# Optimization experiments

Hardware: AMD Instinct MI355X
Metric: run time of the kernel (lower is better)

The kernel has to match this reference:

```python
import jax, jax.numpy as jnp
import numpy as np

N = 100000   # nodes
E = 600000   # edges (before self loops)
D = 128      # dim_latent = H*F
H = 4        # heads
F = 32       # out_feats per head
L = 3        # num GATConv layers (conv_0 + 2)


def setup_inputs() -> dict:
    key = jax.random.key(0)
    ks = jax.random.split(key, 10)
    return {
        "weights": jax.random.normal(ks[0], (N,), jnp.float32),
        "lin_W": jax.random.normal(ks[1], (D, 1), jnp.float32) * 0.1,
        "lin_b": jnp.zeros((D,), jnp.float32),
        "fc_W": jax.random.normal(ks[2], (L, D, D), jnp.float32) * (1.0 / np.sqrt(D)),
        "attn_l": jax.random.normal(ks[3], (L, H, F), jnp.float32) * 0.1,
        "attn_r": jax.random.normal(ks[4], (L, H, F), jnp.float32) * 0.1,
        "conv_b": jnp.zeros((L, D), jnp.float32),
        "pred_W": jax.random.normal(ks[5], (1, D), jnp.float32) * 0.1,
        "pred_b": jnp.zeros((1,), jnp.float32),
        "src": jax.random.randint(ks[6], (E,), 0, N, jnp.int32),
        "dst": jax.random.randint(ks[7], (E,), 0, N, jnp.int32),
    }


def _leaky(x, slope):
    return jnp.where(x >= 0, x, slope * x)


def _gat_conv(x, fc_W, attn_l, attn_r, bias, src, dst):
    # DGL GATConv: bias-free fc, per-head additive attention, edge softmax over dst
    h = (x @ fc_W.T).reshape(N, H, F)                      # [N,H,F]
    el = jnp.sum(h * attn_l[None], axis=-1)                # [N,H]
    er = jnp.sum(h * attn_r[None], axis=-1)                # [N,H]
    e = _leaky(el[src] + er[dst], 0.2)                     # [Etot,H]
    m = jax.ops.segment_max(e, dst, num_segments=N)        # [N,H]
    a = jnp.exp(e - m[dst])                                # [Etot,H]
    s = jax.ops.segment_sum(a, dst, num_segments=N)        # [N,H]
    alpha = a / s[dst]                                     # [Etot,H]
    msg = h[src] * alpha[:, :, None]                       # [Etot,H,F]
    out = jax.ops.segment_sum(msg, dst, num_segments=N)    # [N,H,F]
    out = out + bias.reshape(H, F)[None]
    return out.reshape(N, H * F)


def reference(weights, lin_W, lin_b, fc_W, attn_l, attn_r, conv_b, pred_W, pred_b, src, dst):
    # add self loops (dgl.add_self_loop)
    loop = jnp.arange(N, dtype=src.dtype)
    s_full = jnp.concatenate([src, loop])
    d_full = jnp.concatenate([dst, loop])

    x = weights[:, None] @ lin_W.T + lin_b                 # [N,D]
    for i in range(L):
        if i > 0:
            x = _leaky(x, 0.01)                            # nn.LeakyReLU default
        x = _gat_conv(x, fc_W[i], attn_l[i], attn_r[i], conv_b[i], s_full, d_full)
    logits = x @ pred_W.T + pred_b                         # [N,1]
    return logits
```

## Files before the change

### kernel.cpp

```cpp
#include <hip/hip_runtime.h>
#include <hip/hip_bf16.h>
#include <math.h>


__device__ __forceinline__ float leaky02(float x) {
    return x >= 0.f ? x : 0.2f * x;
}
__device__ __forceinline__ float leaky01(float x) {
    return x >= 0.f ? x : 0.01f * x;
}

__device__ __forceinline__ unsigned short f2bf(float f) {
    unsigned u = __float_as_uint(f);
    unsigned r = u + 0x7FFFu + ((u >> 16) & 1u);
    return (unsigned short)(r >> 16);
}
__device__ __forceinline__ float bf2f(unsigned short s) {
    return __uint_as_float(((unsigned)s) << 16);
}

typedef __attribute__((ext_vector_type(8))) short bf16x8;
typedef __attribute__((ext_vector_type(8))) unsigned short u16x8;
typedef __attribute__((ext_vector_type(4))) float f32x4;

__global__ __launch_bounds__(1024) void prep_kernel(
    int* __restrict__ deg, int N,
    const float* __restrict__ fc_W, const float* __restrict__ attn_l,
    const float* __restrict__ attn_r,
    short* __restrict__ Wh, short* __restrict__ Wl,
    short* __restrict__ Mh, short* __restrict__ Ml,
    const float* __restrict__ lW, const float* __restrict__ lb,
    const float* __restrict__ cb2, const float* __restrict__ pW,
    const float* __restrict__ pb,
    float* __restrict__ c1, float* __restrict__ c2, float* __restrict__ prm)
{
    const int nbi = (N + 1023) >> 10;
    const int b = blockIdx.x;
    const int t = threadIdx.x;

    if (b < nbi) {
        int i = b * 1024 + t;
        if (i < N) deg[i] = 1;
        if (i < 2 * 16384) {
            const float* W = fc_W + 16384;
            int l    = i >> 14;
            int p    = i & 16383;
            int j    = p & 7;
            int lane = (p >> 3) & 63;
            int c    = (p >> 9) & 7;
            int kk   = p >> 12;
            int mr   = lane & 15;
            int quad = lane >> 4;
            int row  = c * 16 + mr;
            int d    = kk * 32 + quad * 8 + j;
            float f = W[(size_t)l * 16384 + row * 128 + d];
            unsigned short hi = f2bf(f);
            Wh[i] = (short)hi;
            Wl[i] = (short)f2bf(f - bf2f(hi));
        }
    } else if (b < nbi + 2) {
        int l = b - nbi;
        const float* W  = fc_W + (size_t)(l + 1) * 16384;
        const float* al = attn_l + (l + 1) * 128;
        const float* ar = attn_r + (l + 1) * 128;
        short* mh = Mh + (size_t)l * 16 * 128;
        short* ml = Ml + (size_t)l * 16 * 128;
        int r = t >> 7;
        int d = t & 127;
        int hh = r & 3;
        const float* av = (r < 4) ? al : ar;
        float s = 0.f;
#pragma unroll
        for (int f = 0; f < 32; ++f)
            s += W[(size_t)(hh * 32 + f) * 128 + d] * av[hh * 32 + f];
        unsigned short hi = f2bf(s);
        mh[r * 128 + d] = (short)hi;
        ml[r * 128 + d] = (short)f2bf(s - bf2f(hi));
        mh[(r + 8) * 128 + d] = 0;
        ml[(r + 8) * 128 + d] = 0;
    } else {
        __shared__ float sh1[128], sh2[128], sh3[128], sh4[128], sh5[128];
        const float* W0 = fc_W;
        const float* al = attn_l;
        const float* ar = attn_r;
        int j = t >> 3, sub = t & 7;
        float s1 = 0.f, s2 = 0.f;
        int d0 = sub * 16;
#pragma unroll
        for (int k = 0; k < 16; ++k) {
            float wv = W0[j * 128 + d0 + k];
            s1 += lW[d0 + k] * wv;
            s2 += lb[d0 + k] * wv;
        }
#pragma unroll
        for (int m = 1; m <= 4; m <<= 1) {
            s1 += __shfl_xor(s1, m, 64);
            s2 += __shfl_xor(s2, m, 64);
        }
        if (sub == 0) {
            c1[j] = s1; c2[j] = s2;
            sh1[j] = s1 * al[j]; sh2[j] = s2 * al[j];
            sh3[j] = s1 * ar[j]; sh4[j] = s2 * ar[j];
            sh5[j] = cb2[j] * pW[j];
        }
        __syncthreads();
        if (t < 4) {
            float p = 0.f, q = 0.f, r = 0.f, s = 0.f;
            for (int f = 0; f < 32; ++f) {
                p += sh1[t * 32 + f]; q += sh2[t * 32 + f];
                r += sh3[t * 32 + f]; s += sh4[t * 32 + f];
            }
            prm[t] = p; prm[4 + t] = q; prm[8 + t] = r; prm[12 + t] = s;
        }
        if (t == 0) {
            float cs = 0.f;
            for (int k = 0; k < 128; ++k) cs += sh5[k];
            prm[16] = cs + pb[0];
        }
    }
}

__global__ __launch_bounds__(256) void deg_count_slot_kernel(
    const int* __restrict__ dst, int* __restrict__ deg,
    int* __restrict__ slot, int E)
{
    int i = blockIdx.x * 256 + threadIdx.x;
    if (i < E) slot[i] = atomicAdd(&deg[dst[i]], 1);
}

#define SCAN_TILE 1024

__global__ __launch_bounds__(256) void scanA_kernel(
    const int* __restrict__ deg, int* __restrict__ bsum, int N)
{
    __shared__ int ws[4];
    int b = blockIdx.x, t = threadIdx.x;
    int base = b * SCAN_TILE + t * 4;
    int s = 0;
#pragma unroll
    for (int k = 0; k < 4; ++k) {
        int i = base + k;
        if (i < N) s += deg[i];
    }
#pragma unroll
    for (int m = 32; m >= 1; m >>= 1) s += __shfl_xor(s, m, 64);
    if ((t & 63) == 0) ws[t >> 6] = s;
    __syncthreads();
    if (t == 0) bsum[b] = ws[0] + ws[1] + ws[2] + ws[3];
}

__global__ __launch_bounds__(1024) void scanB_kernel(
    int* __restrict__ bsum, int* __restrict__ bpre, int* __restrict__ rowp,
    int NB, int N)
{
    __shared__ int sh[1024];
    int t = threadIdx.x;
    int v = (t < NB) ? bsum[t] : 0;
    sh[t] = v;
    __syncthreads();
    for (int off = 1; off < 1024; off <<= 1) {
        int u = (t >= off) ? sh[t - off] : 0;
        __syncthreads();
        sh[t] += u;
        __syncthreads();
    }
    if (t < NB) bpre[t] = sh[t] - v;
    if (t == 1023) rowp[N] = sh[1023];
}

__global__ __launch_bounds__(256) void scanC_kernel(
    const int* __restrict__ deg, const int* __restrict__ bpre,
    int* __restrict__ rowp, int* __restrict__ col, int N)
{
    __shared__ int sh[256];
    int b = blockIdx.x, t = threadIdx.x;
    int base = b * SCAN_TILE + t * 4;
    int v[4];
#pragma unroll
    for (int k = 0; k < 4; ++k) {
        int i = base + k;
        v[k] = (i < N) ? deg[i] : 0;
    }
    int tsum = v[0] + v[1] + v[2] + v[3];
    sh[t] = tsum;
    __syncthreads();
    for (int off = 1; off < 256; off <<= 1) {
        int u = (t >= off) ? sh[t - off] : 0;
        __syncthreads();
        sh[t] += u;
        __syncthreads();
    }
    int pre = bpre[b] + sh[t] - tsum;
#pragma unroll
    for (int k = 0; k < 4; ++k) {
        int i = base + k;
        if (i < N) {
            rowp[i] = pre;
            col[pre] = i;
        }
        pre += v[k];
    }
}

__global__ __launch_bounds__(256) void scatter2_kernel(
    const int* __restrict__ src, const int* __restrict__ dst,
    const int* __restrict__ slot, const int* __restrict__ rowp,
    int* __restrict__ col, int E)
{
    int i = blockIdx.x * 256 + threadIdx.x;
    if (i < E) col[rowp[dst[i]] + slot[i]] = src[i];
}

__global__ __launch_bounds__(256) void agg0_kernel(
    const float* __restrict__ w, const float* __restrict__ c1,
    const float* __restrict__ c2, const float* __restrict__ prm,
    const int* __restrict__ rowp, const int* __restrict__ col,
    const float* __restrict__ bias, unsigned short* __restrict__ xout, int N)
{
    const int lane = threadIdx.x & 63;
    const int q    = lane >> 4;
    const int l16  = lane & 15;
    const int v    = blockIdx.x * 16 + (threadIdx.x >> 6) * 4 + q;
    if (v >= N) return;

    const int r0 = rowp[v], r1 = rowp[v + 1];
    const int head = l16 >> 2;
    const int e4   = l16 & 3;
    const int f0   = l16 * 8;
    const float pl = prm[head],     ql = prm[4 + head];
    const float pr = prm[8 + head], qr = prm[12 + head];

    const float wv  = w[v];
    const float erq = wv * pr + qr;
    const float mref = leaky02(wv * pl + ql + erq);

    float S = 0.f, Sw = 0.f;
    for (int j = r0 + e4; j < r1; j += 4) {
        int u = col[j];
        float wu = w[u];
        float e = leaky02(wu * pl + ql + erq);
        float d = fminf(e - mref, 80.f);
        float p = __expf(d);
        S += p; Sw += p * wu;
    }
    S  += __shfl_xor(S, 1, 64);  S  += __shfl_xor(S, 2, 64);
    Sw += __shfl_xor(Sw, 1, 64); Sw += __shfl_xor(Sw, 2, 64);
    const float t = Sw / S;

    float4 a0 = *reinterpret_cast<const float4*>(&c1[f0]);
    float4 a1 = *reinterpret_cast<const float4*>(&c1[f0 + 4]);
    float4 g0 = *reinterpret_cast<const float4*>(&c2[f0]);
    float4 g1 = *reinterpret_cast<const float4*>(&c2[f0 + 4]);
    float4 b0 = *reinterpret_cast<const float4*>(&bias[f0]);
    float4 b1 = *reinterpret_cast<const float4*>(&bias[f0 + 4]);
    const float aa[8] = {a0.x, a0.y, a0.z, a0.w, a1.x, a1.y, a1.z, a1.w};
    const float gg[8] = {g0.x, g0.y, g0.z, g0.w, g1.x, g1.y, g1.z, g1.w};
    const float bb[8] = {b0.x, b0.y, b0.z, b0.w, b1.x, b1.y, b1.z, b1.w};

    u16x8 o;
#pragma unroll
    for (int k = 0; k < 8; ++k)
        o[k] = f2bf(leaky01(t * aa[k] + gg[k] + bb[k]));
    *reinterpret_cast<u16x8*>(&xout[(size_t)v * 128 + f0]) = o;
}

__global__ __launch_bounds__(256) void gemm_mfma_kernel(
    const unsigned short* __restrict__ xb, const short* __restrict__ Wh,
    const short* __restrict__ Wl, const short* __restrict__ Mh,
    const short* __restrict__ Ml, unsigned short* __restrict__ hb,
    float* __restrict__ el, float* __restrict__ er,
    const float* __restrict__ pW, float* __restrict__ yel,
    int N, int mode)
{
    const int lane = threadIdx.x & 63;
    const int wv   = threadIdx.x >> 6;
    const int m0   = blockIdx.x * 128 + wv * 32;
    const int mr   = lane & 15;
    const int quad = lane >> 4;

    int r0 = m0 + mr;      if (r0 > N - 1) r0 = N - 1;
    int r1 = m0 + 16 + mr; if (r1 > N - 1) r1 = N - 1;
    const unsigned short* xp0 = xb + (size_t)r0 * 128 + quad * 8;
    const unsigned short* xp1 = xb + (size_t)r1 * 128 + quad * 8;

    f32x4 acc0[8], acc1[8], acce0, acce1;
#pragma unroll
    for (int c = 0; c < 8; ++c) {
        acc0[c] = (f32x4){0.f, 0.f, 0.f, 0.f};
        acc1[c] = (f32x4){0.f, 0.f, 0.f, 0.f};
    }
    acce0 = (f32x4){0.f, 0.f, 0.f, 0.f};
    acce1 = (f32x4){0.f, 0.f, 0.f, 0.f};

#pragma unroll
    for (int kk = 0; kk < 4; ++kk) {
        bf16x8 a0 = *reinterpret_cast<const bf16x8*>(xp0 + kk * 32);
        bf16x8 a1 = *reinterpret_cast<const bf16x8*>(xp1 + kk * 32);

        const int kb = kk * 32 + quad * 8;
        bf16x8 bh[8], bl[8];
#pragma unroll
        for (int c = 0; c < 8; ++c) {
            const size_t wo = (size_t)((kk * 8 + c) * 64 + lane) * 8;
            bh[c] = *reinterpret_cast<const bf16x8*>(Wh + wo);
            bl[c] = *reinterpret_cast<const bf16x8*>(Wl + wo);
        }
        bf16x8 eh = *reinterpret_cast<const bf16x8*>(Mh + (size_t)mr * 128 + kb);
        bf16x8 eo = *reinterpret_cast<const bf16x8*>(Ml + (size_t)mr * 128 + kb);
#pragma unroll
        for (int c = 0; c < 8; ++c) {
            acc0[c] = __builtin_amdgcn_mfma_f32_16x16x32_bf16(a0, bh[c], acc0[c], 0, 0, 0);
            acc0[c] = __builtin_amdgcn_mfma_f32_16x16x32_bf16(a0, bl[c], acc0[c], 0, 0, 0);
            acc1[c] = __builtin_amdgcn_mfma_f32_16x16x32_bf16(a1, bh[c], acc1[c], 0, 0, 0);
            acc1[c] = __builtin_amdgcn_mfma_f32_16x16x32_bf16(a1, bl[c], acc1[c], 0, 0, 0);
        }
        acce0 = __builtin_amdgcn_mfma_f32_16x16x32_bf16(a0, eh, acce0, 0, 0, 0);
        acce0 = __builtin_amdgcn_mfma_f32_16x16x32_bf16(a0, eo, acce0, 0, 0, 0);
        acce1 = __builtin_amdgcn_mfma_f32_16x16x32_bf16(a1, eh, acce1, 0, 0, 0);
        acce1 = __builtin_amdgcn_mfma_f32_16x16x32_bf16(a1, eo, acce1, 0, 0, 0);
    }

    if (mode == 0) {
#pragma unroll
        for (int i = 0; i < 4; ++i) {
            int rowA = m0 + quad * 4 + i;
            if (rowA < N) {
                unsigned short* hp = hb + (size_t)rowA * 128 + mr;
#pragma unroll
                for (int c = 0; c < 8; ++c) hp[c * 16] = f2bf(acc0[c][i]);
                if (mr < 4)       el[(size_t)rowA * 4 + mr]       = acce0[i];
                else if (mr < 8)  er[(size_t)rowA * 4 + (mr - 4)] = acce0[i];
            }
            int rowB = m0 + 16 + quad * 4 + i;
            if (rowB < N) {
                unsigned short* hp = hb + (size_t)rowB * 128 + mr;
#pragma unroll
                for (int c = 0; c < 8; ++c) hp[c * 16] = f2bf(acc1[c][i]);
                if (mr < 4)       el[(size_t)rowB * 4 + mr]       = acce1[i];
                else if (mr < 8)  er[(size_t)rowB * 4 + (mr - 4)] = acce1[i];
            }
        }
    } else {
        float pw[8];
#pragma unroll
        for (int c = 0; c < 8; ++c) pw[c] = pW[mr + c * 16];
#pragma unroll
        for (int i = 0; i < 4; ++i) {
            int rowA = m0 + quad * 4 + i;
            {
                float y[4];
#pragma unroll
                for (int h = 0; h < 4; ++h)
                    y[h] = acc0[2 * h][i] * pw[2 * h] + acc0[2 * h + 1][i] * pw[2 * h + 1];
#pragma unroll
                for (int d = 1; d < 16; d <<= 1) {
#pragma unroll
                    for (int h = 0; h < 4; ++h) y[h] += __shfl_xor(y[h], d, 64);
                }
                if (rowA < N) {
                    if (mr < 4) {
                        float2 o; o.x = y[mr]; o.y = acce0[i];
                        *reinterpret_cast<float2*>(&yel[(size_t)rowA * 8 + mr * 2]) = o;
                    } else if (mr < 8) {
                        er[(size_t)rowA * 4 + (mr - 4)] = acce0[i];
                    }
                }
            }
            int rowB = m0 + 16 + quad * 4 + i;
            {
                float y[4];
#pragma unroll
                for (int h = 0; h < 4; ++h)
                    y[h] = acc1[2 * h][i] * pw[2 * h] + acc1[2 * h + 1][i] * pw[2 * h + 1];
#pragma unroll
                for (int d = 1; d < 16; d <<= 1) {
#pragma unroll
                    for (int h = 0; h < 4; ++h) y[h] += __shfl_xor(y[h], d, 64);
                }
                if (rowB < N) {
                    if (mr < 4) {
                        float2 o; o.x = y[mr]; o.y = acce1[i];
                        *reinterpret_cast<float2*>(&yel[(size_t)rowB * 8 + mr * 2]) = o;
                    } else if (mr < 8) {
                        er[(size_t)rowB * 4 + (mr - 4)] = acce1[i];
                    }
                }
            }
        }
    }
}

__global__ __launch_bounds__(256) void agg_mid_kernel(
    const unsigned short* __restrict__ hb, const float* __restrict__ el,
    const float* __restrict__ er, const int* __restrict__ rowp,
    const int* __restrict__ col, const float* __restrict__ bias,
    unsigned short* __restrict__ xout, int N)
{
    const int lane = threadIdx.x & 63;
    const int q    = lane >> 4;
    const int l16  = lane & 15;
    const int v    = blockIdx.x * 16 + (threadIdx.x >> 6) * 4 + q;
    if (v >= N) return;

    const int r0 = rowp[v], r1 = rowp[v + 1];
    const int head = l16 >> 2;
    const int f0   = l16 * 8;
    const float erq = er[(size_t)v * 4 + head];
    const float el_self = el[(size_t)v * 4 + head];
    const float mref = leaky02(el_self + erq);

    float s = 0.f;
    float acc[8];
#pragma unroll
    for (int k = 0; k < 8; ++k) acc[k] = 0.f;

    float elA = el_self;
    u16x8 hvA = *reinterpret_cast<const u16x8*>(&hb[(size_t)v * 128 + f0]);
    int jB = (r0 + 1 < r1) ? r0 + 1 : r1 - 1;
    int uB = col[jB];
    float elB = el[(size_t)uB * 4 + head];
    u16x8 hvB = *reinterpret_cast<const u16x8*>(&hb[(size_t)uB * 128 + f0]);

    for (int j = r0; j < r1; j += 2) {
        int jA2 = (j + 2 < r1) ? j + 2 : r1 - 1;
        int uA2 = col[jA2];
        float elA2 = el[(size_t)uA2 * 4 + head];
        u16x8 hvA2 = *reinterpret_cast<const u16x8*>(&hb[(size_t)uA2 * 128 + f0]);

        {
            float e = leaky02(elA + erq);
            float d = fminf(e - mref, 80.f);
            float p = __expf(d);
            s += p;
#pragma unroll
            for (int k = 0; k < 8; ++k) acc[k] += p * bf2f(hvA[k]);
        }

        if (j + 1 < r1) {
            int jB2 = (j + 3 < r1) ? j + 3 : r1 - 1;
            int uB2 = col[jB2];
            float elB2 = el[(size_t)uB2 * 4 + head];
            u16x8 hvB2 = *reinterpret_cast<const u16x8*>(&hb[(size_t)uB2 * 128 + f0]);

            float e = leaky02(elB + erq);
            float d = fminf(e - mref, 80.f);
            float p = __expf(d);
            s += p;
#pragma unroll
            for (int k = 0; k < 8; ++k) acc[k] += p * bf2f(hvB[k]);

            elB = elB2; hvB = hvB2;
        }
        elA = elA2; hvA = hvA2;
    }
    const float is = 1.f / s;

    float4 b0 = *reinterpret_cast<const float4*>(&bias[f0]);
    float4 b1 = *reinterpret_cast<const float4*>(&bias[f0 + 4]);
    const float bb[8] = {b0.x, b0.y, b0.z, b0.w, b1.x, b1.y, b1.z, b1.w};

    u16x8 o;
#pragma unroll
    for (int k = 0; k < 8; ++k) o[k] = f2bf(leaky01(acc[k] * is + bb[k]));
    *reinterpret_cast<u16x8*>(&xout[(size_t)v * 128 + f0]) = o;
}

__global__ __launch_bounds__(256) void agg2_kernel(
    const float* __restrict__ yel, const float* __restrict__ er,
    const int* __restrict__ rowp, const int* __restrict__ col,
    const float* __restrict__ prm, float* __restrict__ logits, int N)
{
    const int lane = threadIdx.x & 63;
    const int q    = lane >> 4;
    const int l16  = lane & 15;
    const int v    = blockIdx.x * 16 + (threadIdx.x >> 6) * 4 + q;
    if (v >= N) return;

    const int r0 = rowp[v], r1 = rowp[v + 1];
    const int head = l16 >> 2;
    const int e4   = l16 & 3;
    const float erq = er[(size_t)v * 4 + head];

    float2 selfy = *reinterpret_cast<const float2*>(&yel[(size_t)v * 8 + head * 2]);
    const float mref = leaky02(selfy.y + erq);

    float S = 0.f, A = 0.f;
    for (int j = r0 + e4; j < r1; j += 4) {
        int u = col[j];
        float2 c = *reinterpret_cast<const float2*>(&yel[(size_t)u * 8 + head * 2]);
        float e = leaky02(c.y + erq);
        float d = fminf(e - mref, 80.f);
        float p = __expf(d);
        S += p; A += p * c.x;
    }
    S += __shfl_xor(S, 1, 64); S += __shfl_xor(S, 2, 64);
    A += __shfl_xor(A, 1, 64); A += __shfl_xor(A, 2, 64);
    float part = A / S;
    part += __shfl_xor(part, 4, 64);
    part += __shfl_xor(part, 8, 64);
    if (l16 == 0) logits[v] = part + prm[16];
}

extern "C" void kernel_launch(void* const* d_in, const int* in_sizes, int n_in,
                              void* d_out, int out_size, void* d_ws, size_t ws_size,
                              hipStream_t stream)
{
    const float* weights = (const float*)d_in[0];
    const float* lin_W   = (const float*)d_in[1];
    const float* lin_b   = (const float*)d_in[2];
    const float* fc_W    = (const float*)d_in[3];
    const float* attn_l  = (const float*)d_in[4];
    const float* attn_r  = (const float*)d_in[5];
    const float* conv_b  = (const float*)d_in[6];
    const float* pred_W  = (const float*)d_in[7];
    const float* pred_b  = (const float*)d_in[8];
    const int*   src     = (const int*)d_in[9];
    const int*   dst     = (const int*)d_in[10];

    const int N = in_sizes[0];
    const int E = in_sizes[9];
    const int NB = (N + SCAN_TILE - 1) / SCAN_TILE;
    const int NBI = (N + 1023) / 1024;

    unsigned short* xb = (unsigned short*)d_ws;
    unsigned short* hb = xb + (size_t)N * 128;
    float* el  = (float*)(hb + (size_t)N * 128);
    float* er  = el + (size_t)N * 4;
    float* yel = er + (size_t)N * 4;
    float* c1  = yel + (size_t)N * 8;
    float* c2  = c1 + 128;
    float* prm = c2 + 128;
    short* Whs = (short*)(prm + 32);
    short* Wls = Whs + 2 * 16384;
    short* Mhs = Wls + 2 * 16384;
    short* Mls = Mhs + 2 * 2048;
    int*   deg  = (int*)(Mls + 2 * 2048);
    int*   rowp = deg + N;
    int*   slot = rowp + (N + 1);
    int*   col  = slot + E;
    int*   bsum = col + (E + N);
    int*   bpre = bsum + NB;

    prep_kernel<<<NBI + 3, 1024, 0, stream>>>(
        deg, N, fc_W, attn_l, attn_r, Whs, Wls, Mhs, Mls,
        lin_W, lin_b, conv_b + 2 * 128, pred_W, pred_b, c1, c2, prm);

    deg_count_slot_kernel<<<(E + 255) / 256, 256, 0, stream>>>(dst, deg, slot, E);
    scanA_kernel<<<NB, 256, 0, stream>>>(deg, bsum, N);
    scanB_kernel<<<1, 1024, 0, stream>>>(bsum, bpre, rowp, NB, N);
    scanC_kernel<<<NB, 256, 0, stream>>>(deg, bpre, rowp, col, N);
    scatter2_kernel<<<(E + 255) / 256, 256, 0, stream>>>(src, dst, slot, rowp, col, E);

    agg0_kernel<<<(N + 15) / 16, 256, 0, stream>>>(
        weights, c1, c2, prm, rowp, col, conv_b, xb, N);

    gemm_mfma_kernel<<<(N + 127) / 128, 256, 0, stream>>>(
        xb, Whs, Wls, Mhs, Mls, hb, el, er, pred_W, yel, N, 0);
    agg_mid_kernel<<<(N + 15) / 16, 256, 0, stream>>>(
        hb, el, er, rowp, col, conv_b + 128, xb, N);

    gemm_mfma_kernel<<<(N + 127) / 128, 256, 0, stream>>>(
        xb, Whs + 16384, Wls + 16384, Mhs + 2048, Mls + 2048,
        hb, el, er, pred_W, yel, N, 1);
    agg2_kernel<<<(N + 15) / 16, 256, 0, stream>>>(
        yel, er, rowp, col, prm, (float*)d_out, N);
}
```

Before: 251.8 us.

## Fuse edge aggregation into following GEMM and collapse scan into single pass

Each aggregation stage now writes its bf16 node features into a shared-memory tile, and the same block immediately runs the MFMA projection for the next layer. This removes the global round trip of the intermediate feature matrix and two kernel launches. The three-kernel prefix scan is replaced by one kernel in which each 1024-node block claims its output base with an atomic counter. CSR row offsets are therefore no longer ordered by vertex, so row ends are computed from deg instead of rowp[v+1]. The trade-off is that each block now aggregates 128 nodes serially across 8 passes before its GEMM can start, which may reduce latency hiding.

```diff
diff --git a/kernel.cpp b/kernel.cpp
--- a/kernel.cpp
+++ b/kernel.cpp
@@ -32,11 +32,13 @@
     const float* __restrict__ lW, const float* __restrict__ lb,
     const float* __restrict__ cb2, const float* __restrict__ pW,
     const float* __restrict__ pb,
-    float* __restrict__ c1, float* __restrict__ c2, float* __restrict__ prm)
+    float* __restrict__ c1, float* __restrict__ c2, float* __restrict__ prm,
+    int* __restrict__ base_ctr)
 {
     const int nbi = (N + 1023) >> 10;
     const int b = blockIdx.x;
     const int t = threadIdx.x;
+    if (b == 0 && t == 0) *base_ctr = 0;
 
     if (b < nbi) {
         int i = b * 1024 + t;
@@ -128,34 +130,15 @@
     if (i < E) slot[i] = atomicAdd(&deg[dst[i]], 1);
 }
 
-#define SCAN_TILE 1024
-
-__global__ __launch_bounds__(256) void scanA_kernel(
-    const int* __restrict__ deg, int* __restrict__ bsum, int N)
-{
-    __shared__ int ws[4];
+__global__ __launch_bounds__(1024) void scan_kernel(
+    const int* __restrict__ deg, int* __restrict__ base_ctr,
+    int* __restrict__ rowp, int* __restrict__ col, int N)
+{
+    __shared__ int sh[1024];
+    __shared__ int sbase;
     int b = blockIdx.x, t = threadIdx.x;
-    int base = b * SCAN_TILE + t * 4;
-    int s = 0;
-#pragma unroll
-    for (int k = 0; k < 4; ++k) {
-        int i = base + k;
-        if (i < N) s += deg[i];
-    }
-#pragma unroll
-    for (int m = 32; m >= 1; m >>= 1) s += __shfl_xor(s, m, 64);
-    if ((t & 63) == 0) ws[t >> 6] = s;
-    __syncthreads();
-    if (t == 0) bsum[b] = ws[0] + ws[1] + ws[2] + ws[3];
-}
-
-__global__ __launch_bounds__(1024) void scanB_kernel(
-    int* __restrict__ bsum, int* __restrict__ bpre, int* __restrict__ rowp,
-    int NB, int N)
-{
-    __shared__ int sh[1024];
-    int t = threadIdx.x;
-    int v = (t < NB) ? bsum[t] : 0;
+    int i = b * 1024 + t;
+    int v = (i < N) ? deg[i] : 0;
     sh[t] = v;
     __syncthreads();
     for (int off = 1; off < 1024; off <<= 1) {
@@ -164,41 +147,12 @@
         sh[t] += u;
         __syncthreads();
     }
-    if (t < NB) bpre[t] = sh[t] - v;
-    if (t == 1023) rowp[N] = sh[1023];
-}
-
-__global__ __launch_bounds__(256) void scanC_kernel(
-    const int* __restrict__ deg, const int* __restrict__ bpre,
-    int* __restrict__ rowp, int* __restrict__ col, int N)
-{
-    __shared__ int sh[256];
-    int b = blockIdx.x, t = threadIdx.x;
-    int base = b * SCAN_TILE + t * 4;
-    int v[4];
-#pragma unroll
-    for (int k = 0; k < 4; ++k) {
-        int i = base + k;
-        v[k] = (i < N) ? deg[i] : 0;
-    }
-    int tsum = v[0] + v[1] + v[2] + v[3];
-    sh[t] = tsum;
+    if (t == 1023) sbase = atomicAdd(base_ctr, sh[1023]);
     __syncthreads();
-    for (int off = 1; off < 256; off <<= 1) {
-        int u = (t >= off) ? sh[t - off] : 0;
-        __syncthreads();
-        sh[t] += u;
-        __syncthreads();
-    }
-    int pre = bpre[b] + sh[t] - tsum;
-#pragma unroll
-    for (int k = 0; k < 4; ++k) {
-        int i = base + k;
-        if (i < N) {
-            rowp[i] = pre;
-            col[pre] = i;
-        }
-        pre += v[k];
+    int pre = sbase + sh[t] - v;
+    if (i < N) {
+        rowp[i] = pre;
+        col[pre] = i;
     }
 }
 
@@ -211,11 +165,319 @@
     if (i < E) col[rowp[dst[i]] + slot[i]] = src[i];
 }
 
-__global__ __launch_bounds__(256) void agg0_kernel(
+__global__ __launch_bounds__(256) void l0g1_kernel(
     const float* __restrict__ w, const float* __restrict__ c1,
     const float* __restrict__ c2, const float* __restrict__ prm,
-    const int* __restrict__ rowp, const int* __restrict__ col,
-    const float* __restrict__ bias, unsigned short* __restrict__ xout, int N)
+    const int* __restrict__ rowp, const int* __restrict__ deg,
+    const int* __restrict__ col, const float* __restrict__ bias,
+    const short* __restrict__ Wh, const short* __restrict__ Wl,
+    const short* __restrict__ Mh, const short* __restrict__ Ml,
+    unsigned short* __restrict__ hb, float* __restrict__ el,
+    float* __restrict__ er, int N)
+{
+    __shared__ unsigned short xs[128][136];
+    const int t    = threadIdx.x;
+    const int lane = t & 63;
+    const int wv   = t >> 6;
+    const int q    = lane >> 4;
+    const int l16  = lane & 15;
+    const int head = l16 >> 2;
+    const int e4   = l16 & 3;
+    const int f0   = l16 * 8;
+    const int vbase = blockIdx.x * 128;
+
+    const float pl = prm[head],     ql = prm[4 + head];
+    const float pr = prm[8 + head], qr = prm[12 + head];
+    float4 a0v = *reinterpret_cast<const float4*>(&c1[f0]);
+    float4 a1v = *reinterpret_cast<const float4*>(&c1[f0 + 4]);
+    float4 g0v = *reinterpret_cast<const float4*>(&c2[f0]);
+    float4 g1v = *reinterpret_cast<const float4*>(&c2[f0 + 4]);
+    float4 b0v = *reinterpret_cast<const float4*>(&bias[f0]);
+    float4 b1v = *reinterpret_cast<const float4*>(&bias[f0 + 4]);
+    const float aa[8] = {a0v.x, a0v.y, a0v.z, a0v.w, a1v.x, a1v.y, a1v.z, a1v.w};
+    const float gg[8] = {g0v.x, g0v.y, g0v.z, g0v.w, g1v.x, g1v.y, g1v.z, g1v.w};
+    const float bb[8] = {b0v.x, b0v.y, b0v.z, b0v.w, b1v.x, b1v.y, b1v.z, b1v.w};
+
+#pragma unroll
+    for (int p = 0; p < 8; ++p) {
+        const int lr = p * 16 + wv * 4 + q;
+        const int v  = vbase + lr;
+        u16x8 o;
+        if (v < N) {
+            const int r0 = rowp[v];
+            const int r1 = r0 + deg[v];
+            const float wvx  = w[v];
+            const float erq  = wvx * pr + qr;
+            const float mref = leaky02(wvx * pl + ql + erq);
+            float S = 0.f, Sw = 0.f;
+            for (int j = r0 + e4; j < r1; j += 4) {
+                int u = col[j];
+                float wu = w[u];
+                float e = leaky02(wu * pl + ql + erq);
+                float d = fminf(e - mref, 80.f);
+                float pp = __expf(d);
+                S += pp; Sw += pp * wu;
+            }
+            S  += __shfl_xor(S, 1, 64);  S  += __shfl_xor(S, 2, 64);
+            Sw += __shfl_xor(Sw, 1, 64); Sw += __shfl_xor(Sw, 2, 64);
+            const float tt = Sw / S;
+#pragma unroll
+            for (int k = 0; k < 8; ++k)
+                o[k] = f2bf(leaky01(tt * aa[k] + gg[k] + bb[k]));
+        } else {
+#pragma unroll
+            for (int k = 0; k < 8; ++k) o[k] = 0;
+        }
+        *reinterpret_cast<u16x8*>(&xs[lr][f0]) = o;
+    }
+    __syncthreads();
+
+    const int m0   = vbase + wv * 32;
+    const int mr   = lane & 15;
+    const int quad = lane >> 4;
+
+    f32x4 acc0[8], acc1[8], acce0, acce1;
+#pragma unroll
+    for (int c = 0; c < 8; ++c) {
+        acc0[c] = (f32x4){0.f, 0.f, 0.f, 0.f};
+        acc1[c] = (f32x4){0.f, 0.f, 0.f, 0.f};
+    }
+    acce0 = (f32x4){0.f, 0.f, 0.f, 0.f};
+    acce1 = (f32x4){0.f, 0.f, 0.f, 0.f};
+
+#pragma unroll
+    for (int kk = 0; kk < 4; ++kk) {
+        bf16x8 a0 = *reinterpret_cast<const bf16x8*>(&xs[wv * 32 + mr][quad * 8 + kk * 32]);
+        bf16x8 a1 = *reinterpret_cast<const bf16x8*>(&xs[wv * 32 + 16 + mr][quad * 8 + kk * 32]);
+
+        const int kb = kk * 32 + quad * 8;
+        bf16x8 bh[8], bl[8];
+#pragma unroll
+        for (int c = 0; c < 8; ++c) {
+            const size_t wo = (size_t)((kk * 8 + c) * 64 + lane) * 8;
+            bh[c] = *reinterpret_cast<const bf16x8*>(Wh + wo);
+            bl[c] = *reinterpret_cast<const bf16x8*>(Wl + wo);
+        }
+        bf16x8 eh = *reinterpret_cast<const bf16x8*>(Mh + (size_t)mr * 128 + kb);
+        bf16x8 eo = *reinterpret_cast<const bf16x8*>(Ml + (size_t)mr * 128 + kb);
+#pragma unroll
+        for (int c = 0; c < 8; ++c) {
+            acc0[c] = __builtin_amdgcn_mfma_f32_16x16x32_bf16(a0, bh[c], acc0[c], 0, 0, 0);
+            acc0[c] = __builtin_amdgcn_mfma_f32_16x16x32_bf16(a0, bl[c], acc0[c], 0, 0, 0);
+            acc1[c] = __builtin_amdgcn_mfma_f32_16x16x32_bf16(a1, bh[c], acc1[c], 0, 0, 0);
+            acc1[c] = __builtin_amdgcn_mfma_f32_16x16x32_bf16(a1, bl[c], acc1[c], 0, 0, 0);
+        }
+        acce0 = __builtin_amdgcn_mfma_f32_16x16x32_bf16(a0, eh, acce0, 0, 0, 0);
+        acce0 = __builtin_amdgcn_mfma_f32_16x16x32_bf16(a0, eo, acce0, 0, 0, 0);
+        acce1 = __builtin_amdgcn_mfma_f32_16x16x32_bf16(a1, eh, acce1, 0, 0, 0);
+        acce1 = __builtin_amdgcn_mfma_f32_16x16x32_bf16(a1, eo, acce1, 0, 0, 0);
+    }
+
+#pragma unroll
+    for (int i = 0; i < 4; ++i) {
+        int rowA = m0 + quad * 4 + i;
+        if (rowA < N) {
+            unsigned short* hp = hb + (size_t)rowA * 128 + mr;
+#pragma unroll
+            for (int c = 0; c < 8; ++c) hp[c * 16] = f2bf(acc0[c][i]);
+            if (mr < 4)       el[(size_t)rowA * 4 + mr]       = acce0[i];
+            else if (mr < 8)  er[(size_t)rowA * 4 + (mr - 4)] = acce0[i];
+        }
+        int rowB = m0 + 16 + quad * 4 + i;
+        if (rowB < N) {
+            unsigned short* hp = hb + (size_t)rowB * 128 + mr;
+#pragma unroll
+            for (int c = 0; c < 8; ++c) hp[c * 16] = f2bf(acc1[c][i]);
+            if (mr < 4)       el[(size_t)rowB * 4 + mr]       = acce1[i];
+            else if (mr < 8)  er[(size_t)rowB * 4 + (mr - 4)] = acce1[i];
+        }
+    }
+}
+
+__global__ __launch_bounds__(256) void midg2_kernel(
+    const unsigned short* __restrict__ hb, const float* __restrict__ el,
+    float* __restrict__ er, const int* __restrict__ rowp,
+    const int* __restrict__ deg, const int* __restrict__ col,
+    const float* __restrict__ bias,
+    const short* __restrict__ Wh, const short* __restrict__ Wl,
+    const short* __restrict__ Mh, const short* __restrict__ Ml,
+    const float* __restrict__ pW, float* __restrict__ yel, int N)
+{
+    __shared__ unsigned short xs[128][136];
+    const int t    = threadIdx.x;
+    const int lane = t & 63;
+    const int wv   = t >> 6;
+    const int q    = lane >> 4;
+    const int l16  = lane & 15;
+    const int head = l16 >> 2;
+    const int f0   = l16 * 8;
+    const int vbase = blockIdx.x * 128;
+
+    float4 b0v = *reinterpret_cast<const float4*>(&bias[f0]);
+    float4 b1v = *reinterpret_cast<const float4*>(&bias[f0 + 4]);
+    const float bb[8] = {b0v.x, b0v.y, b0v.z, b0v.w, b1v.x, b1v.y, b1v.z, b1v.w};
+
+#pragma unroll
+    for (int p = 0; p < 8; ++p) {
+        const int lr = p * 16 + wv * 4 + q;
+        const int v  = vbase + lr;
+        u16x8 o;
+        if (v < N) {
+            const int r0 = rowp[v];
+            const int r1 = r0 + deg[v];
+            const float erq = er[(size_t)v * 4 + head];
+            const float el_self = el[(size_t)v * 4 + head];
+            const float mref = leaky02(el_self + erq);
+
+            float s = 0.f;
+            float acc[8];
+#pragma unroll
+            for (int k = 0; k < 8; ++k) acc[k] = 0.f;
+
+            float elA = el_self;
+            u16x8 hvA = *reinterpret_cast<const u16x8*>(&hb[(size_t)v * 128 + f0]);
+            int jB = (r0 + 1 < r1) ? r0 + 1 : r1 - 1;
+            int uB = col[jB];
+            float elB = el[(size_t)uB * 4 + head];
+            u16x8 hvB = *reinterpret_cast<const u16x8*>(&hb[(size_t)uB * 128 + f0]);
+
+            for (int j = r0; j < r1; j += 2) {
+                int jA2 = (j + 2 < r1) ? j + 2 : r1 - 1;
+                int uA2 = col[jA2];
+                float elA2 = el[(size_t)uA2 * 4 + head];
+                u16x8 hvA2 = *reinterpret_cast<const u16x8*>(&hb[(size_t)uA2 * 128 + f0]);
+
+                {
+                    float e = leaky02(elA + erq);
+                    float d = fminf(e - mref, 80.f);
+                    float pp = __expf(d);
+                    s += pp;
+#pragma unroll
+                    for (int k = 0; k < 8; ++k) acc[k] += pp * bf2f(hvA[k]);
+                }
+                if (j + 1 < r1) {
+                    int jB2 = (j + 3 < r1) ? j + 3 : r1 - 1;
+                    int uB2 = col[jB2];
+                    float elB2 = el[(size_t)uB2 * 4 + head];
+                    u16x8 hvB2 = *reinterpret_cast<const u16x8*>(&hb[(size_t)uB2 * 128 + f0]);
+
+                    float e = leaky02(elB + erq);
+                    float d = fminf(e - mref, 80.f);
+                    float pp = __expf(d);
+                    s += pp;
+#pragma unroll
+                    for (int k = 0; k < 8; ++k) acc[k] += pp * bf2f(hvB[k]);
+
+                    elB = elB2; hvB = hvB2;
+                }
+                elA = elA2; hvA = hvA2;
+            }
+            const float is = 1.f / s;
+#pragma unroll
+            for (int k = 0; k < 8; ++k)
+                o[k] = f2bf(leaky01(acc[k] * is + bb[k]));
+        } else {
+#pragma unroll
+            for (int k = 0; k < 8; ++k) o[k] = 0;
+        }
+        *reinterpret_cast<u16x8*>(&xs[lr][f0]) = o;
+    }
+    __syncthreads();
+
+    const int m0   = vbase + wv * 32;
+    const int mr   = lane & 15;
+    const int quad = lane >> 4;
+
+    f32x4 acc0[8], acc1[8], acce0, acce1;
+#pragma unroll
+    for (int c = 0; c < 8; ++c) {
+        acc0[c] = (f32x4){0.f, 0.f, 0.f, 0.f};
+        acc1[c] = (f32x4){0.f, 0.f, 0.f, 0.f};
+    }
+    acce0 = (f32x4){0.f, 0.f, 0.f, 0.f};
+    acce1 = (f32x4){0.f, 0.f, 0.f, 0.f};
+
+#pragma unroll
+    for (int kk = 0; kk < 4; ++kk) {
+        bf16x8 a0 = *reinterpret_cast<const bf16x8*>(&xs[wv * 32 + mr][quad * 8 + kk * 32]);
+        bf16x8 a1 = *reinterpret_cast<const bf16x8*>(&xs[wv * 32 + 16 + mr][quad * 8 + kk * 32]);
+
+        const int kb = kk * 32 + quad * 8;
+        bf16x8 bh[8], bl[8];
+#pragma unroll
+        for (int c = 0; c < 8; ++c) {
+            const size_t wo = (size_t)((kk * 8 + c) * 64 + lane) * 8;
+            bh[c] = *reinterpret_cast<const bf16x8*>(Wh + wo);
+            bl[c] = *reinterpret_cast<const bf16x8*>(Wl + wo);
+        }
+        bf16x8 eh = *reinterpret_cast<const bf16x8*>(Mh + (size_t)mr * 128 + kb);
+        bf16x8 eo = *reinterpret_cast<const bf16x8*>(Ml + (size_t)mr * 128 + kb);
+#pragma unroll
+        for (int c = 0; c < 8; ++c) {
+            acc0[c] = __builtin_amdgcn_mfma_f32_16x16x32_bf16(a0, bh[c], acc0[c], 0, 0, 0);
+            acc0[c] = __builtin_amdgcn_mfma_f32_16x16x32_bf16(a0, bl[c], acc0[c], 0, 0, 0);
+            acc1[c] = __builtin_amdgcn_mfma_f32_16x16x32_bf16(a1, bh[c], acc1[c], 0, 0, 0);
+            acc1[c] = __builtin_amdgcn_mfma_f32_16x16x32_bf16(a1, bl[c], acc1[c], 0, 0, 0);
+        }
+        acce0 = __builtin_amdgcn_mfma_f32_16x16x32_bf16(a0, eh, acce0, 0, 0, 0);
+        acce0 = __builtin_amdgcn_mfma_f32_16x16x32_bf16(a0, eo, acce0, 0, 0, 0);
+        acce1 = __builtin_amdgcn_mfma_f32_16x16x32_bf16(a1, eh, acce1, 0, 0, 0);
+        acce1 = __builtin_amdgcn_mfma_f32_16x16x32_bf16(a1, eo, acce1, 0, 0, 0);
+    }
+
+    float pw[8];
+#pragma unroll
+    for (int c = 0; c < 8; ++c) pw[c] = pW[mr + c * 16];
+#pragma unroll
+    for (int i = 0; i < 4; ++i) {
+        int rowA = m0 + quad * 4 + i;
+        {
+            float y[4];
+#pragma unroll
+            for (int h = 0; h < 4; ++h)
+                y[h] = acc0[2 * h][i] * pw[2 * h] + acc0[2 * h + 1][i] * pw[2 * h + 1];
+#pragma unroll
+            for (int d = 1; d < 16; d <<= 1) {
+#pragma unroll
+                for (int h = 0; h < 4; ++h) y[h] += __shfl_xor(y[h], d, 64);
+            }
+            if (rowA < N) {
+                if (mr < 4) {
+                    float2 o; o.x = y[mr]; o.y = acce0[i];
+                    *reinterpret_cast<float2*>(&yel[(size_t)rowA * 8 + mr * 2]) = o;
+                } else if (mr < 8) {
+                    er[(size_t)rowA * 4 + (mr - 4)] = acce0[i];
+                }
+            }
+        }
+        int rowB = m0 + 16 + quad * 4 + i;
+        {
+            float y[4];
+#pragma unroll
+            for (int h = 0; h < 4; ++h)
+                y[h] = acc1[2 * h][i] * pw[2 * h] + acc1[2 * h + 1][i] * pw[2 * h + 1];
+#pragma unroll
+            for (int d = 1; d < 16; d <<= 1) {
+#pragma unroll
+                for (int h = 0; h < 4; ++h) y[h] += __shfl_xor(y[h], d, 64);
+            }
+            if (rowB < N) {
+                if (mr < 4) {
+                    float2 o; o.x = y[mr]; o.y = acce1[i];
+                    *reinterpret_cast<float2*>(&yel[(size_t)rowB * 8 + mr * 2]) = o;
+                } else if (mr < 8) {
+                    er[(size_t)rowB * 4 + (mr - 4)] = acce1[i];
+                }
+            }
+        }
+    }
+}
+
+__global__ __launch_bounds__(256) void agg2_kernel(
+    const float* __restrict__ yel, const float* __restrict__ er,
+    const int* __restrict__ rowp, const int* __restrict__ deg,
+    const int* __restrict__ col, const float* __restrict__ prm,
+    float* __restrict__ logits, int N)
 {
     const int lane = threadIdx.x & 63;
     const int q    = lane >> 4;
@@ -223,260 +485,8 @@
     const int v    = blockIdx.x * 16 + (threadIdx.x >> 6) * 4 + q;
     if (v >= N) return;
 
-    const int r0 = rowp[v], r1 = rowp[v + 1];
-    const int head = l16 >> 2;
-    const int e4   = l16 & 3;
-    const int f0   = l16 * 8;
-    const float pl = prm[head],     ql = prm[4 + head];
-    const float pr = prm[8 + head], qr = prm[12 + head];
-
-    const float wv  = w[v];
-    const float erq = wv * pr + qr;
-    const float mref = leaky02(wv * pl + ql + erq);
-
-    float S = 0.f, Sw = 0.f;
-    for (int j = r0 + e4; j < r1; j += 4) {
-        int u = col[j];
-        float wu = w[u];
-        float e = leaky02(wu * pl + ql + erq);
-        float d = fminf(e - mref, 80.f);
-        float p = __expf(d);
-        S += p; Sw += p * wu;
-    }
-    S  += __shfl_xor(S, 1, 64);  S  += __shfl_xor(S, 2, 64);
-    Sw += __shfl_xor(Sw, 1, 64); Sw += __shfl_xor(Sw, 2, 64);
-    const float t = Sw / S;
-
-    float4 a0 = *reinterpret_cast<const float4*>(&c1[f0]);
-    float4 a1 = *reinterpret_cast<const float4*>(&c1[f0 + 4]);
-    float4 g0 = *reinterpret_cast<const float4*>(&c2[f0]);
-    float4 g1 = *reinterpret_cast<const float4*>(&c2[f0 + 4]);
-    float4 b0 = *reinterpret_cast<const float4*>(&bias[f0]);
-    float4 b1 = *reinterpret_cast<const float4*>(&bias[f0 + 4]);
-    const float aa[8] = {a0.x, a0.y, a0.z, a0.w, a1.x, a1.y, a1.z, a1.w};
-    const float gg[8] = {g0.x, g0.y, g0.z, g0.w, g1.x, g1.y, g1.z, g1.w};
-    const float bb[8] = {b0.x, b0.y, b0.z, b0.w, b1.x, b1.y, b1.z, b1.w};
-
-    u16x8 o;
-#pragma unroll
-    for (int k = 0; k < 8; ++k)
-        o[k] = f2bf(leaky01(t * aa[k] + gg[k] + bb[k]));
-    *reinterpret_cast<u16x8*>(&xout[(size_t)v * 128 + f0]) = o;
-}
-
-__global__ __launch_bounds__(256) void gemm_mfma_kernel(
-    const unsigned short* __restrict__ xb, const short* __restrict__ Wh,
-    const short* __restrict__ Wl, const short* __restrict__ Mh,
-    const short* __restrict__ Ml, unsigned short* __restrict__ hb,
-    float* __restrict__ el, float* __restrict__ er,
-    const float* __restrict__ pW, float* __restrict__ yel,
-    int N, int mode)
-{
-    const int lane = threadIdx.x & 63;
-    const int wv   = threadIdx.x >> 6;
-    const int m0   = blockIdx.x * 128 + wv * 32;
-    const int mr   = lane & 15;
-    const int quad = lane >> 4;
-
-    int r0 = m0 + mr;      if (r0 > N - 1) r0 = N - 1;
-    int r1 = m0 + 16 + mr; if (r1 > N - 1) r1 = N - 1;
-    const unsigned short* xp0 = xb + (size_t)r0 * 128 + quad * 8;
-    const unsigned short* xp1 = xb + (size_t)r1 * 128 + quad * 8;
-
-    f32x4 acc0[8], acc1[8], acce0, acce1;
-#pragma unroll
-    for (int c = 0; c < 8; ++c) {
-        acc0[c] = (f32x4){0.f, 0.f, 0.f, 0.f};
-        acc1[c] = (f32x4){0.f, 0.f, 0.f, 0.f};
-    }
-    acce0 = (f32x4){0.f, 0.f, 0.f, 0.f};
-    acce1 = (f32x4){0.f, 0.f, 0.f, 0.f};
-
-#pragma unroll
-    for (int kk = 0; kk < 4; ++kk) {
-        bf16x8 a0 = *reinterpret_cast<const bf16x8*>(xp0 + kk * 32);
-        bf16x8 a1 = *reinterpret_cast<const bf16x8*>(xp1 + kk * 32);
-
-        const int kb = kk * 32 + quad * 8;
-        bf16x8 bh[8], bl[8];
-#pragma unroll
-        for (int c = 0; c < 8; ++c) {
-            const size_t wo = (size_t)((kk * 8 + c) * 64 + lane) * 8;
-            bh[c] = *reinterpret_cast<const bf16x8*>(Wh + wo);
-            bl[c] = *reinterpret_cast<const bf16x8*>(Wl + wo);
-        }
-        bf16x8 eh = *reinterpret_cast<const bf16x8*>(Mh + (size_t)mr * 128 + kb);
-        bf16x8 eo = *reinterpret_cast<const bf16x8*>(Ml + (size_t)mr * 128 + kb);
-#pragma unroll
-        for (int c = 0; c < 8; ++c) {
-            acc0[c] = __builtin_amdgcn_mfma_f32_16x16x32_bf16(a0, bh[c], acc0[c], 0, 0, 0);
-            acc0[c] = __builtin_amdgcn_mfma_f32_16x16x32_bf16(a0, bl[c], acc0[c], 0, 0, 0);
-            acc1[c] = __builtin_amdgcn_mfma_f32_16x16x32_bf16(a1, bh[c], acc1[c], 0, 0, 0);
-            acc1[c] = __builtin_amdgcn_mfma_f32_16x16x32_bf16(a1, bl[c], acc1[c], 0, 0, 0);
-        }
-        acce0 = __builtin_amdgcn_mfma_f32_16x16x32_bf16(a0, eh, acce0, 0, 0, 0);
-        acce0 = __builtin_amdgcn_mfma_f32_16x16x32_bf16(a0, eo, acce0, 0, 0, 0);
-        acce1 = __builtin_amdgcn_mfma_f32_16x16x32_bf16(a1, eh, acce1, 0, 0, 0);
-        acce1 = __builtin_amdgcn_mfma_f32_16x16x32_bf16(a1, eo, acce1, 0, 0, 0);
-    }
-
-    if (mode == 0) {
-#pragma unroll
-        for (int i = 0; i < 4; ++i) {
-            int rowA = m0 + quad * 4 + i;
-            if (rowA < N) {
-                unsigned short* hp = hb + (size_t)rowA * 128 + mr;
-#pragma unroll
-                for (int c = 0; c < 8; ++c) hp[c * 16] = f2bf(acc0[c][i]);
-                if (mr < 4)       el[(size_t)rowA * 4 + mr]       = acce0[i];
-                else if (mr < 8)  er[(size_t)rowA * 4 + (mr - 4)] = acce0[i];
-            }
-            int rowB = m0 + 16 + quad * 4 + i;
-            if (rowB < N) {
-                unsigned short* hp = hb + (size_t)rowB * 128 + mr;
-#pragma unroll
-                for (int c = 0; c < 8; ++c) hp[c * 16] = f2bf(acc1[c][i]);
-                if (mr < 4)       el[(size_t)rowB * 4 + mr]       = acce1[i];
-                else if (mr < 8)  er[(size_t)rowB * 4 + (mr - 4)] = acce1[i];
-            }
-        }
-    } else {
-        float pw[8];
-#pragma unroll
-        for (int c = 0; c < 8; ++c) pw[c] = pW[mr + c * 16];
-#pragma unroll
-        for (int i = 0; i < 4; ++i) {
-            int rowA = m0 + quad * 4 + i;
-            {
-                float y[4];
-#pragma unroll
-                for (int h = 0; h < 4; ++h)
-                    y[h] = acc0[2 * h][i] * pw[2 * h] + acc0[2 * h + 1][i] * pw[2 * h + 1];
-#pragma unroll
-                for (int d = 1; d < 16; d <<= 1) {
-#pragma unroll
-                    for (int h = 0; h < 4; ++h) y[h] += __shfl_xor(y[h], d, 64);
-                }
-                if (rowA < N) {
-                    if (mr < 4) {
-                        float2 o; o.x = y[mr]; o.y = acce0[i];
-                        *reinterpret_cast<float2*>(&yel[(size_t)rowA * 8 + mr * 2]) = o;
-                    } else if (mr < 8) {
-                        er[(size_t)rowA * 4 + (mr - 4)] = acce0[i];
-                    }
-                }
-            }
-            int rowB = m0 + 16 + quad * 4 + i;
-            {
-                float y[4];
-#pragma unroll
-                for (int h = 0; h < 4; ++h)
-                    y[h] = acc1[2 * h][i] * pw[2 * h] + acc1[2 * h + 1][i] * pw[2 * h + 1];
-#pragma unroll
-                for (int d = 1; d < 16; d <<= 1) {
-#pragma unroll
-                    for (int h = 0; h < 4; ++h) y[h] += __shfl_xor(y[h], d, 64);
-                }
-                if (rowB < N) {
-                    if (mr < 4) {
-                        float2 o; o.x = y[mr]; o.y = acce1[i];
-                        *reinterpret_cast<float2*>(&yel[(size_t)rowB * 8 + mr * 2]) = o;
-                    } else if (mr < 8) {
-                        er[(size_t)rowB * 4 + (mr - 4)] = acce1[i];
-                    }
-                }
-            }
-        }
-    }
-}
-
-__global__ __launch_bounds__(256) void agg_mid_kernel(
-    const unsigned short* __restrict__ hb, const float* __restrict__ el,
-    const float* __restrict__ er, const int* __restrict__ rowp,
-    const int* __restrict__ col, const float* __restrict__ bias,
-    unsigned short* __restrict__ xout, int N)
-{
-    const int lane = threadIdx.x & 63;
-    const int q    = lane >> 4;
-    const int l16  = lane & 15;
-    const int v    = blockIdx.x * 16 + (threadIdx.x >> 6) * 4 + q;
-    if (v >= N) return;
-
-    const int r0 = rowp[v], r1 = rowp[v + 1];
-    const int head = l16 >> 2;
-    const int f0   = l16 * 8;
-    const float erq = er[(size_t)v * 4 + head];
-    const float el_self = el[(size_t)v * 4 + head];
-    const float mref = leaky02(el_self + erq);
-
-    float s = 0.f;
-    float acc[8];
-#pragma unroll
-    for (int k = 0; k < 8; ++k) acc[k] = 0.f;
-
-    float elA = el_self;
-    u16x8 hvA = *reinterpret_cast<const u16x8*>(&hb[(size_t)v * 128 + f0]);
-    int jB = (r0 + 1 < r1) ? r0 + 1 : r1 - 1;
-    int uB = col[jB];
-    float elB = el[(size_t)uB * 4 + head];
-    u16x8 hvB = *reinterpret_cast<const u16x8*>(&hb[(size_t)uB * 128 + f0]);
-
-    for (int j = r0; j < r1; j += 2) {
-        int jA2 = (j + 2 < r1) ? j + 2 : r1 - 1;
-        int uA2 = col[jA2];
-        float elA2 = el[(size_t)uA2 * 4 + head];
-        u16x8 hvA2 = *reinterpret_cast<const u16x8*>(&hb[(size_t)uA2 * 128 + f0]);
-
-        {
-            float e = leaky02(elA + erq);
-            float d = fminf(e - mref, 80.f);
-            float p = __expf(d);
-            s += p;
-#pragma unroll
-            for (int k = 0; k < 8; ++k) acc[k] += p * bf2f(hvA[k]);
-        }
-
-        if (j + 1 < r1) {
-            int jB2 = (j + 3 < r1) ? j + 3 : r1 - 1;
-            int uB2 = col[jB2];
-            float elB2 = el[(size_t)uB2 * 4 + head];
-            u16x8 hvB2 = *reinterpret_cast<const u16x8*>(&hb[(size_t)uB2 * 128 + f0]);
-
-            float e = leaky02(elB + erq);
-            float d = fminf(e - mref, 80.f);
-            float p = __expf(d);
-            s += p;
-#pragma unroll
-            for (int k = 0; k < 8; ++k) acc[k] += p * bf2f(hvB[k]);
-
-            elB = elB2; hvB = hvB2;
-        }
-        elA = elA2; hvA = hvA2;
-    }
-    const float is = 1.f / s;
-
-    float4 b0 = *reinterpret_cast<const float4*>(&bias[f0]);
-    float4 b1 = *reinterpret_cast<const float4*>(&bias[f0 + 4]);
-    const float bb[8] = {b0.x, b0.y, b0.z, b0.w, b1.x, b1.y, b1.z, b1.w};
-
-    u16x8 o;
-#pragma unroll
-    for (int k = 0; k < 8; ++k) o[k] = f2bf(leaky01(acc[k] * is + bb[k]));
-    *reinterpret_cast<u16x8*>(&xout[(size_t)v * 128 + f0]) = o;
-}
-
-__global__ __launch_bounds__(256) void agg2_kernel(
-    const float* __restrict__ yel, const float* __restrict__ er,
-    const int* __restrict__ rowp, const int* __restrict__ col,
-    const float* __restrict__ prm, float* __restrict__ logits, int N)
-{
-    const int lane = threadIdx.x & 63;
-    const int q    = lane >> 4;
-    const int l16  = lane & 15;
-    const int v    = blockIdx.x * 16 + (threadIdx.x >> 6) * 4 + q;
-    if (v >= N) return;
-
-    const int r0 = rowp[v], r1 = rowp[v + 1];
+    const int r0 = rowp[v];
+    const int r1 = r0 + deg[v];
     const int head = l16 >> 2;
     const int e4   = l16 & 3;
     const float erq = er[(size_t)v * 4 + head];
@@ -519,11 +529,9 @@
 
     const int N = in_sizes[0];
     const int E = in_sizes[9];
-    const int NB = (N + SCAN_TILE - 1) / SCAN_TILE;
-    const int NBI = (N + 1023) / 1024;
-
-    unsigned short* xb = (unsigned short*)d_ws;
-    unsigned short* hb = xb + (size_t)N * 128;
+    const int NB1024 = (N + 1023) / 1024;
+
+    unsigned short* hb = (unsigned short*)d_ws;
     float* el  = (float*)(hb + (size_t)N * 128);
     float* er  = el + (size_t)N * 4;
     float* yel = er + (size_t)N * 4;
@@ -538,30 +546,26 @@
     int*   rowp = deg + N;
     int*   slot = rowp + (N + 1);
     int*   col  = slot + E;
-    int*   bsum = col + (E + N);
-    int*   bpre = bsum + NB;
-
-    prep_kernel<<<NBI + 3, 1024, 0, stream>>>(
+    int*   bctr = col + (E + N);
+
+    prep_kernel<<<NB1024 + 3, 1024, 0, stream>>>(
         deg, N, fc_W, attn_l, attn_r, Whs, Wls, Mhs, Mls,
-        lin_W, lin_b, conv_b + 2 * 128, pred_W, pred_b, c1, c2, prm);
+        lin_W, lin_b, conv_b + 2 * 128, pred_W, pred_b, c1, c2, prm, bctr);
 
     deg_count_slot_kernel<<<(E + 255) / 256, 256, 0, stream>>>(dst, deg, slot, E);
-    scanA_kernel<<<NB, 256, 0, stream>>>(deg, bsum, N);
-    scanB_kernel<<<1, 1024, 0, stream>>>(bsum, bpre, rowp, NB, N);
-    scanC_kernel<<<NB, 256, 0, stream>>>(deg, bpre, rowp, col, N);
+
+    scan_kernel<<<NB1024, 1024, 0, stream>>>(deg, bctr, rowp, col, N);
+
     scatter2_kernel<<<(E + 255) / 256, 256, 0, stream>>>(src, dst, slot, rowp, col, E);
 
-    agg0_kernel<<<(N + 15) / 16, 256, 0, stream>>>(
-        weights, c1, c2, prm, rowp, col, conv_b, xb, N);
-
-    gemm_mfma_kernel<<<(N + 127) / 128, 256, 0, stream>>>(
-        xb, Whs, Wls, Mhs, Mls, hb, el, er, pred_W, yel, N, 0);
-    agg_mid_kernel<<<(N + 15) / 16, 256, 0, stream>>>(
-        hb, el, er, rowp, col, conv_b + 128, xb, N);
-
-    gemm_mfma_kernel<<<(N + 127) / 128, 256, 0, stream>>>(
-        xb, Whs + 16384, Wls + 16384, Mhs + 2048, Mls + 2048,
-        hb, el, er, pred_W, yel, N, 1);
+    l0g1_kernel<<<(N + 127) / 128, 256, 0, stream>>>(
+        weights, c1, c2, prm, rowp, deg, col, conv_b,
+        Whs, Wls, Mhs, Mls, hb, el, er, N);
+
+    midg2_kernel<<<(N + 127) / 128, 256, 0, stream>>>(
+        hb, el, er, rowp, deg, col, conv_b + 128,
+        Whs + 16384, Wls + 16384, Mhs + 2048, Mls + 2048, pred_W, yel, N);
+
     agg2_kernel<<<(N + 15) / 16, 256, 0, stream>>>(
-        yel, er, rowp, col, prm, (float*)d_out, N);
-}
+        yel, er, rowp, deg, col, prm, (float*)d_out, N);
+}
```

Result: slower. 296.5 us (+17.8%).
